# Kernel optimization log

Hardware: AMD Instinct MI355X
Metric: run time of the kernel (lower is better)

Reference implementation:

```python
import jax, jax.numpy as jnp
import numpy as np

N = 100000
E = 1600000
D_IN, D_HID, D_OUT = 256, 256, 128


def _sage_conv(x, src, dst, Wl, bl, Wr, n_nodes):
    # PyG SAGEConv (aggr='mean'): out = lin_l(mean_{j in N(i)} x_j) + lin_r(x_i)
    msg = x[src]                                               # [E, d]
    summed = jax.ops.segment_sum(msg, dst, num_segments=n_nodes)  # [N, d]
    deg = jax.ops.segment_sum(jnp.ones((src.shape[0],), x.dtype), dst,
                              num_segments=n_nodes)            # [N]
    agg = summed / jnp.maximum(deg, 1.0)[:, None]              # mean, 0 if isolated
    return agg @ Wl.T + bl + x @ Wr.T


def setup_inputs() -> dict:
    key = jax.random.key(0)
    ks = jax.random.split(key, 8)
    x = jax.random.normal(ks[0], (N, D_IN), dtype=jnp.float32)
    edge_index = jax.random.randint(ks[1], (2, E), 0, N, dtype=jnp.int32)
    s1 = 1.0 / np.sqrt(D_IN)
    s2 = 1.0 / np.sqrt(D_HID)
    W1l = jax.random.uniform(ks[2], (D_HID, D_IN), jnp.float32, -s1, s1)
    b1 = jnp.zeros((D_HID,), jnp.float32)
    W1r = jax.random.uniform(ks[3], (D_HID, D_IN), jnp.float32, -s1, s1)
    W2l = jax.random.uniform(ks[4], (D_OUT, D_HID), jnp.float32, -s2, s2)
    b2 = jnp.zeros((D_OUT,), jnp.float32)
    W2r = jax.random.uniform(ks[5], (D_OUT, D_HID), jnp.float32, -s2, s2)
    return {"x": x, "edge_index": edge_index, "W1l": W1l, "b1": b1,
            "W1r": W1r, "W2l": W2l, "b2": b2, "W2r": W2r}


def reference(x, edge_index, W1l, b1, W1r, W2l, b2, W2r):
    src, dst = edge_index[0], edge_index[1]
    h = _sage_conv(x, src, dst, W1l, b1, W1r, x.shape[0])
    h = jax.nn.relu(h)
    out = _sage_conv(h, src, dst, W2l, b2, W2r, x.shape[0])
    return out
```

## Files before the change

### kernel.cpp

```cpp
#include <hip/hip_runtime.h>

#define DK 256
#define BN 256
#define NBLK 512

typedef __attribute__((ext_vector_type(8))) short bf16x8;
typedef __attribute__((ext_vector_type(4))) float f32x4;

__device__ __forceinline__ unsigned short f2b(float f) {
    unsigned u = __builtin_bit_cast(unsigned, f);
    u += 0x7FFFu + ((u >> 16) & 1u);
    return (unsigned short)(u >> 16);
}
__device__ __forceinline__ float b2f(unsigned short s) {
    return __builtin_bit_cast(float, (unsigned)s << 16);
}
__device__ __forceinline__ void gld_lds16(void* lds, const void* g) {
    __builtin_amdgcn_global_load_lds(
        (const __attribute__((address_space(1))) unsigned int*)g,
        (__attribute__((address_space(3))) unsigned int*)lds, 16, 0, 0);
}

__global__ __launch_bounds__(256) void k_cvt(const float* __restrict__ src,
                                             unsigned short* __restrict__ dst, int n4) {
    int i = blockIdx.x * 256 + threadIdx.x;
    if (i < n4) {
        float4 v = reinterpret_cast<const float4*>(src)[i];
        ushort4 o = make_ushort4(f2b(v.x), f2b(v.y), f2b(v.z), f2b(v.w));
        reinterpret_cast<ushort4*>(dst)[i] = o;
    }
}

__global__ __launch_bounds__(256) void k_scan_a(const int* __restrict__ in,
                                                int* __restrict__ bsum, int N) {
    __shared__ int sm[256];
    int t = threadIdx.x;
    int i0 = blockIdx.x * 1024 + t * 4;
    int s = 0;
    if (i0 + 3 < N) {
        int4 v = *reinterpret_cast<const int4*>(in + i0);
        s = v.x + v.y + v.z + v.w;
    } else {
        for (int i = i0; i < min(i0 + 4, N); ++i) s += in[i];
    }
    sm[t] = s;
    __syncthreads();
    for (int off = 128; off > 0; off >>= 1) {
        if (t < off) sm[t] += sm[t + off];
        __syncthreads();
    }
    if (t == 0) bsum[blockIdx.x] = sm[0];
}

__global__ __launch_bounds__(256) void k_scan_b(const int* __restrict__ bsum,
                                                int* __restrict__ boff,
                                                int* __restrict__ totN, int NB) {
    __shared__ int sm[256];
    int t = threadIdx.x;
    sm[t] = (t < NB) ? bsum[t] : 0;
    __syncthreads();
    for (int off = 1; off < 256; off <<= 1) {
        int v = (t >= off) ? sm[t - off] : 0;
        __syncthreads();
        sm[t] += v;
        __syncthreads();
    }
    if (t < NB) boff[t] = (t == 0) ? 0 : sm[t - 1];
    if (t == NB - 1) *totN = sm[t];
}

__global__ __launch_bounds__(256) void k_scan_c(const int* __restrict__ in,
                                                const int* __restrict__ boff,
                                                int* __restrict__ rowptr,
                                                float* __restrict__ invdeg, int N) {
    __shared__ int sm[256];
    int t = threadIdx.x;
    int i0 = blockIdx.x * 1024 + t * 4;
    int d0 = 0, d1 = 0, d2 = 0, d3 = 0;
    if (i0 + 3 < N) {
        int4 v = *reinterpret_cast<const int4*>(in + i0);
        d0 = v.x; d1 = v.y; d2 = v.z; d3 = v.w;
    } else {
        if (i0 + 0 < N) d0 = in[i0 + 0];
        if (i0 + 1 < N) d1 = in[i0 + 1];
        if (i0 + 2 < N) d2 = in[i0 + 2];
        if (i0 + 3 < N) d3 = in[i0 + 3];
    }
    int s = d0 + d1 + d2 + d3;
    sm[t] = s;
    __syncthreads();
    for (int off = 1; off < 256; off <<= 1) {
        int v = (t >= off) ? sm[t - off] : 0;
        __syncthreads();
        sm[t] += v;
        __syncthreads();
    }
    int run = boff[blockIdx.x] + sm[t] - s;
    int dd[4] = {d0, d1, d2, d3};
#pragma unroll
    for (int i = 0; i < 4; ++i) {
        int idx = i0 + i;
        if (idx < N) {
            rowptr[idx] = run;
            invdeg[idx] = 1.0f / fmaxf((float)dd[i], 1.0f);
            run += dd[i];
        }
    }
}

__global__ __launch_bounds__(256) void k_scan_c2(const int* __restrict__ in,
                                                 const int* __restrict__ boff,
                                                 int* __restrict__ outx, int N) {
    __shared__ int sm[256];
    int t = threadIdx.x;
    int i0 = blockIdx.x * 1024 + t * 4;
    int d0 = 0, d1 = 0, d2 = 0, d3 = 0;
    if (i0 + 3 < N) {
        int4 v = *reinterpret_cast<const int4*>(in + i0);
        d0 = v.x; d1 = v.y; d2 = v.z; d3 = v.w;
    } else {
        if (i0 + 0 < N) d0 = in[i0 + 0];
        if (i0 + 1 < N) d1 = in[i0 + 1];
        if (i0 + 2 < N) d2 = in[i0 + 2];
        if (i0 + 3 < N) d3 = in[i0 + 3];
    }
    int s = d0 + d1 + d2 + d3;
    sm[t] = s;
    __syncthreads();
    for (int off = 1; off < 256; off <<= 1) {
        int v = (t >= off) ? sm[t - off] : 0;
        __syncthreads();
        sm[t] += v;
        __syncthreads();
    }
    int run = boff[blockIdx.x] + sm[t] - s;
    int dd[4] = {d0, d1, d2, d3};
#pragma unroll
    for (int i = 0; i < 4; ++i) {
        int idx = i0 + i;
        if (idx < N) { outx[idx] = run; run += dd[i]; }
    }
}

__global__ __launch_bounds__(256) void k_hist(const int* __restrict__ dst,
                                              int* __restrict__ hist,
                                              int E, int NBUK) {
    extern __shared__ int h[];
    int t = threadIdx.x;
    for (int b = t; b < NBUK; b += 256) h[b] = 0;
    __syncthreads();
    int CH = (E + NBLK - 1) / NBLK;
    int beg = blockIdx.x * CH;
    int end = min(beg + CH, E);
    for (int i = beg + t; i < end; i += 256)
        atomicAdd(&h[dst[i] >> 8], 1);
    __syncthreads();
    for (int b = t; b < NBUK; b += 256)
        hist[b * NBLK + blockIdx.x] = h[b];
}

__global__ __launch_bounds__(256) void k_part(const int* __restrict__ src,
                                              const int* __restrict__ dst,
                                              const int* __restrict__ hoff,
                                              unsigned* __restrict__ scratch,
                                              int E, int NBUK) {
    extern __shared__ int cur[];
    int t = threadIdx.x;
    for (int b = t; b < NBUK; b += 256) cur[b] = hoff[b * NBLK + blockIdx.x];
    __syncthreads();
    int CH = (E + NBLK - 1) / NBLK;
    int beg = blockIdx.x * CH;
    int end = min(beg + CH, E);
    for (int i = beg + t; i < end; i += 256) {
        int d = dst[i];
        int p = atomicAdd(&cur[d >> 8], 1);
        scratch[p] = (unsigned)src[i] | ((unsigned)(d & 255) << 20);
    }
}

__global__ __launch_bounds__(256) void k_degb(const unsigned* __restrict__ scratch,
                                              const int* __restrict__ hoff,
                                              int* __restrict__ degi,
                                              int E, int NBUK, int N) {
    __shared__ int cnt[BN];
    int b = blockIdx.x;
    int t = threadIdx.x;
    cnt[t] = 0;
    __syncthreads();
    int beg = hoff[b * NBLK];
    int end = (b + 1 < NBUK) ? hoff[(b + 1) * NBLK] : E;
    for (int i = beg + t; i < end; i += 256)
        atomicAdd(&cnt[scratch[i] >> 20], 1);
    __syncthreads();
    int node = b * BN + t;
    if (node < N) degi[node] = cnt[t];
}

__global__ __launch_bounds__(256) void k_scatter2(const unsigned* __restrict__ scratch,
                                                  const int* __restrict__ hoff,
                                                  const int* __restrict__ rowptr,
                                                  int* __restrict__ col,
                                                  int E, int NBUK, int N) {
    __shared__ int cur[BN];
    int b = blockIdx.x;
    int t = threadIdx.x;
    int node = b * BN + t;
    if (node < N) cur[t] = rowptr[node];
    __syncthreads();
    int beg = hoff[b * NBLK];
    int end = (b + 1 < NBUK) ? hoff[(b + 1) * NBLK] : E;
    for (int i = beg + t; i < end; i += 256) {
        unsigned v = scratch[i];
        int p = atomicAdd(&cur[v >> 20], 1);
        col[p] = (int)(v & 0xFFFFFu);
    }
}

template <bool RF32>
__global__ __launch_bounds__(256) void k_gemm_bf16(const unsigned short* __restrict__ A,
                                                   const unsigned short* __restrict__ W,
                                                   unsigned short* __restrict__ Y,
                                                   void* __restrict__ Rv,
                                                   int DOUTA, int N) {
    __shared__ unsigned short As[128 * 32];
    __shared__ unsigned short Bs[128 * 32];
    const int tid  = threadIdx.x;
    const int lane = tid & 63;
    const int w    = tid >> 6;
    const int wm   = w & 1, wn = w >> 1;
    const int m0   = blockIdx.x * 128;
    const int n0   = blockIdx.y * 128;
    const int lm   = lane & 15, quad = lane >> 4;

    f32x4 acc[4][4];
#pragma unroll
    for (int i = 0; i < 4; ++i)
#pragma unroll
        for (int j = 0; j < 4; ++j) acc[i][j] = (f32x4){0.f, 0.f, 0.f, 0.f};

    const int srow  = lane >> 2;
    const int skoff = (lane & 3) * 8;
    const int ca = 2 * w, cb = 2 * w + 1;

    for (int k0 = 0; k0 < DK; k0 += 32) {
        int ra = min(m0 + 16 * ca + srow, N - 1);
        int rb = min(m0 + 16 * cb + srow, N - 1);
        gld_lds16(As + ca * 512, A + (size_t)ra * DK + k0 + skoff);
        gld_lds16(As + cb * 512, A + (size_t)rb * DK + k0 + skoff);
        int na = n0 + 16 * ca + srow;
        int nb = n0 + 16 * cb + srow;
        gld_lds16(Bs + ca * 512, W + (size_t)na * DK + k0 + skoff);
        gld_lds16(Bs + cb * 512, W + (size_t)nb * DK + k0 + skoff);
        __syncthreads();

        bf16x8 af[4], bfr[4];
#pragma unroll
        for (int mt = 0; mt < 4; ++mt)
            af[mt] = *reinterpret_cast<const bf16x8*>(As + (wm * 64 + mt * 16 + lm) * 32 + quad * 8);
#pragma unroll
        for (int nt = 0; nt < 4; ++nt)
            bfr[nt] = *reinterpret_cast<const bf16x8*>(Bs + (wn * 64 + nt * 16 + lm) * 32 + quad * 8);
#pragma unroll
        for (int mt = 0; mt < 4; ++mt)
#pragma unroll
            for (int nt = 0; nt < 4; ++nt)
                acc[mt][nt] = __builtin_amdgcn_mfma_f32_16x16x32_bf16(af[mt], bfr[nt], acc[mt][nt], 0, 0, 0);
        __syncthreads();
    }

    const bool yPart = (n0 < DOUTA);
#pragma unroll
    for (int mt = 0; mt < 4; ++mt) {
#pragma unroll
        for (int nt = 0; nt < 4; ++nt) {
            int gn = n0 + wn * 64 + nt * 16 + lm;
#pragma unroll
            for (int reg = 0; reg < 4; ++reg) {
                int gm = m0 + wm * 64 + mt * 16 + quad * 4 + reg;
                if (gm < N) {
                    float v = acc[mt][nt][reg];
                    if (yPart) {
                        Y[(size_t)gm * DOUTA + gn] = f2b(v);
                    } else if (RF32) {
                        ((float*)Rv)[(size_t)gm * DOUTA + (gn - DOUTA)] = v;
                    } else {
                        ((unsigned short*)Rv)[(size_t)gm * DOUTA + (gn - DOUTA)] = f2b(v);
                    }
                }
            }
        }
    }
}

__global__ __launch_bounds__(256) void k_agg256(const unsigned short* __restrict__ Y,
                                                const unsigned short* __restrict__ Rb,
                                                const float* __restrict__ bias,
                                                const float* __restrict__ invdeg,
                                                const int* __restrict__ rowptr,
                                                const int* __restrict__ col,
                                                unsigned short* __restrict__ H, int N) {
    long long g = (long long)blockIdx.x * 256 + threadIdx.x;
    int node = (int)(g >> 6);
    int lane = (int)(g & 63);
    if (node >= N) return;
    int beg = rowptr[node], end = rowptr[node + 1];
    const unsigned short* yb = Y + lane * 4;
    float a0 = 0, a1 = 0, a2 = 0, a3 = 0;
    int e = beg;
    for (; e + 7 < end; e += 8) {
        int s[8];
#pragma unroll
        for (int u = 0; u < 8; ++u) s[u] = col[e + u];
        ushort4 v[8];
#pragma unroll
        for (int u = 0; u < 8; ++u)
            v[u] = *reinterpret_cast<const ushort4*>(yb + (size_t)s[u] * 256);
#pragma unroll
        for (int u = 0; u < 8; ++u) {
            a0 += b2f(v[u].x);
            a1 += b2f(v[u].y);
            a2 += b2f(v[u].z);
            a3 += b2f(v[u].w);
        }
    }
    for (; e < end; ++e) {
        ushort4 v0 = *reinterpret_cast<const ushort4*>(yb + (size_t)col[e] * 256);
        a0 += b2f(v0.x); a1 += b2f(v0.y); a2 += b2f(v0.z); a3 += b2f(v0.w);
    }
    float inv = invdeg[node];
    int c = lane * 4;
    ushort4 r = *reinterpret_cast<const ushort4*>(Rb + (size_t)node * 256 + c);
    float o0 = fmaxf(a0 * inv + bias[c + 0] + b2f(r.x), 0.f);
    float o1 = fmaxf(a1 * inv + bias[c + 1] + b2f(r.y), 0.f);
    float o2 = fmaxf(a2 * inv + bias[c + 2] + b2f(r.z), 0.f);
    float o3 = fmaxf(a3 * inv + bias[c + 3] + b2f(r.w), 0.f);
    *reinterpret_cast<ushort4*>(H + (size_t)node * 256 + c) =
        make_ushort4(f2b(o0), f2b(o1), f2b(o2), f2b(o3));
}

__global__ __launch_bounds__(256) void k_agg128(const unsigned short* __restrict__ Y,
                                                const float* __restrict__ Rf,
                                                const float* __restrict__ bias,
                                                const float* __restrict__ invdeg,
                                                const int* __restrict__ rowptr,
                                                const int* __restrict__ col,
                                                float* __restrict__ O, int N) {
    long long g = (long long)blockIdx.x * 256 + threadIdx.x;
    int node = (int)(g >> 6);
    int lane = (int)(g & 63);
    if (node >= N) return;
    int beg = rowptr[node], end = rowptr[node + 1];
    const unsigned short* yb = Y + lane * 2;
    float a0 = 0, a1 = 0;
    int e = beg;
    for (; e + 7 < end; e += 8) {
        int s[8];
#pragma unroll
        for (int u = 0; u < 8; ++u) s[u] = col[e + u];
        unsigned v[8];
#pragma unroll
        for (int u = 0; u < 8; ++u)
            v[u] = *reinterpret_cast<const unsigned*>(yb + (size_t)s[u] * 128);
#pragma unroll
        for (int u = 0; u < 8; ++u) {
            a0 += b2f((unsigned short)(v[u] & 0xffff));
            a1 += b2f((unsigned short)(v[u] >> 16));
        }
    }
    for (; e < end; ++e) {
        unsigned v0 = *reinterpret_cast<const unsigned*>(yb + (size_t)col[e] * 128);
        a0 += b2f((unsigned short)(v0 & 0xffff));
        a1 += b2f((unsigned short)(v0 >> 16));
    }
    float inv = invdeg[node];
    int c = lane * 2;
    float2 r = *reinterpret_cast<const float2*>(Rf + (size_t)node * 128 + c);
    float2 o;
    o.x = a0 * inv + bias[c + 0] + r.x;
    o.y = a1 * inv + bias[c + 1] + r.y;
    *reinterpret_cast<float2*>(O + (size_t)node * 128 + c) = o;
}

extern "C" void kernel_launch(void* const* d_in, const int* in_sizes, int n_in,
                              void* d_out, int out_size, void* d_ws, size_t ws_size,
                              hipStream_t stream) {
    const float* x   = (const float*)d_in[0];
    const int*   ei  = (const int*)d_in[1];
    const float* W1l = (const float*)d_in[2];
    const float* b1  = (const float*)d_in[3];
    const float* W1r = (const float*)d_in[4];
    const float* W2l = (const float*)d_in[5];
    const float* b2  = (const float*)d_in[6];
    const float* W2r = (const float*)d_in[7];
    float* out = (float*)d_out;

    const int N = in_sizes[0] / DK;
    const int E = in_sizes[1] / 2;
    const int* src = ei;
    const int* dst = ei + E;

    unsigned short* xb  = (unsigned short*)d_ws;
    unsigned short* y1b = xb + (size_t)N * 256;
    unsigned short* r1b = y1b + (size_t)N * 256;
    unsigned short* hb  = r1b + (size_t)N * 256;
    unsigned short* Wb1 = hb + (size_t)N * 256;
    unsigned short* Wb2 = Wb1 + 512 * 256;
    float* invdeg = (float*)(Wb2 + 256 * 256);
    int* degi   = (int*)(invdeg + N);
    int* rowptr = degi + N;
    int* col    = rowptr + (N + 1);
    int* bsum   = col + E;
    int* boff   = bsum + 512;
    unsigned short* y2b = y1b;
    float* r2f = (float*)r1b;

    const int NBUK = (N + BN - 1) / BN;
    const int NH   = NBUK * NBLK;
    unsigned* scratch = (unsigned*)hb;
    int* hist  = (int*)y1b;
    int* hoff  = hist + NH;
    int* bsum2 = hoff + NH;
    int* boff2 = bsum2 + 512;
    int* tot2  = boff2 + 512;

    k_cvt<<<(N * 64 + 255) / 256, 256, 0, stream>>>(x, xb, N * 64);
    k_cvt<<<(16384 + 255) / 256, 256, 0, stream>>>(W1l, Wb1, 16384);
    k_cvt<<<(16384 + 255) / 256, 256, 0, stream>>>(W1r, Wb1 + 256 * 256, 16384);
    k_cvt<<<(8192 + 255) / 256, 256, 0, stream>>>(W2l, Wb2, 8192);
    k_cvt<<<(8192 + 255) / 256, 256, 0, stream>>>(W2r, Wb2 + 128 * 256, 8192);

    const int NB2 = (NH + 1023) / 1024;
    const int NB  = (N + 1023) / 1024;
    k_hist<<<NBLK, 256, NBUK * sizeof(int), stream>>>(dst, hist, E, NBUK);
    k_scan_a<<<NB2, 256, 0, stream>>>(hist, bsum2, NH);
    k_scan_b<<<1, 256, 0, stream>>>(bsum2, boff2, tot2, NB2);
    k_scan_c2<<<NB2, 256, 0, stream>>>(hist, boff2, hoff, NH);
    k_part<<<NBLK, 256, NBUK * sizeof(int), stream>>>(src, dst, hoff, scratch, E, NBUK);
    k_degb<<<NBUK, 256, 0, stream>>>(scratch, hoff, degi, E, NBUK, N);
    k_scan_a<<<NB, 256, 0, stream>>>(degi, bsum, N);
    k_scan_b<<<1, 256, 0, stream>>>(bsum, boff, rowptr + N, NB);
    k_scan_c<<<NB, 256, 0, stream>>>(degi, boff, rowptr, invdeg, N);
    k_scatter2<<<NBUK, 256, 0, stream>>>(scratch, hoff, rowptr, col, E, NBUK, N);

    int mTiles = (N + 127) / 128;
    int aggBlocks = (N + 3) / 4;

    k_gemm_bf16<false><<<dim3(mTiles, 4), 256, 0, stream>>>(xb, Wb1, y1b, r1b, 256, N);
    k_agg256<<<aggBlocks, 256, 0, stream>>>(y1b, r1b, b1, invdeg, rowptr, col, hb, N);

    k_gemm_bf16<true><<<dim3(mTiles, 2), 256, 0, stream>>>(hb, Wb2, y2b, r2f, 128, N);
    k_agg128<<<aggBlocks, 256, 0, stream>>>(y2b, r2f, b2, invdeg, rowptr, col, out, N);
}
```

Measured before the change: 539.9 us.

## Widen aggregation loads with half-wave edge split, loop N-tiles in GEMM, merge weight casts

Both aggregation kernels now give each half-wave its own edges and use wider per-lane loads (16 bytes for the 256-wide layer, 8 bytes for the 128-wide one). The two halves are combined with a cross-half shuffle, and the bias and residual are read as vectors. The GEMMs drop the grid y-dimension and loop over output column tiles inside one block, so the A tile rows stay hot in cache across N-tiles, at the cost of fewer blocks. The four weight-conversion launches are merged into one kernel to cut launch overhead.

```diff
diff --git a/kernel.cpp b/kernel.cpp
--- a/kernel.cpp
+++ b/kernel.cpp
@@ -29,6 +29,24 @@
         ushort4 o = make_ushort4(f2b(v.x), f2b(v.y), f2b(v.z), f2b(v.w));
         reinterpret_cast<ushort4*>(dst)[i] = o;
     }
+}
+
+__global__ __launch_bounds__(256) void k_cvtw(const float* __restrict__ a,
+                                              const float* __restrict__ b,
+                                              const float* __restrict__ c,
+                                              const float* __restrict__ d,
+                                              unsigned short* __restrict__ Wb1,
+                                              unsigned short* __restrict__ Wb2) {
+    int i = blockIdx.x * 256 + threadIdx.x;
+    const float* s;
+    unsigned short* o;
+    if (i < 16384)      { s = a; o = Wb1; }
+    else if (i < 32768) { s = b; o = Wb1 + 256 * 256; i -= 16384; }
+    else if (i < 40960) { s = c; o = Wb2;             i -= 32768; }
+    else                { s = d; o = Wb2 + 128 * 256; i -= 40960; }
+    float4 v = reinterpret_cast<const float4*>(s)[i];
+    ushort4 w = make_ushort4(f2b(v.x), f2b(v.y), f2b(v.z), f2b(v.w));
+    reinterpret_cast<ushort4*>(o)[i] = w;
 }
 
 __global__ __launch_bounds__(256) void k_scan_a(const int* __restrict__ in,
@@ -216,12 +234,12 @@
     }
 }
 
-template <bool RF32>
+template <bool RF32, int NT>
 __global__ __launch_bounds__(256) void k_gemm_bf16(const unsigned short* __restrict__ A,
                                                    const unsigned short* __restrict__ W,
                                                    unsigned short* __restrict__ Y,
-                                                   void* __restrict__ Rv,
-                                                   int DOUTA, int N) {
+                                                   void* __restrict__ Rv, int N) {
+    constexpr int DOUTA = NT * 64;
     __shared__ unsigned short As[128 * 32];
     __shared__ unsigned short Bs[128 * 32];
     const int tid  = threadIdx.x;
@@ -229,62 +247,64 @@
     const int w    = tid >> 6;
     const int wm   = w & 1, wn = w >> 1;
     const int m0   = blockIdx.x * 128;
-    const int n0   = blockIdx.y * 128;
     const int lm   = lane & 15, quad = lane >> 4;
-
-    f32x4 acc[4][4];
-#pragma unroll
-    for (int i = 0; i < 4; ++i)
-#pragma unroll
-        for (int j = 0; j < 4; ++j) acc[i][j] = (f32x4){0.f, 0.f, 0.f, 0.f};
 
     const int srow  = lane >> 2;
     const int skoff = (lane & 3) * 8;
     const int ca = 2 * w, cb = 2 * w + 1;
 
-    for (int k0 = 0; k0 < DK; k0 += 32) {
-        int ra = min(m0 + 16 * ca + srow, N - 1);
-        int rb = min(m0 + 16 * cb + srow, N - 1);
-        gld_lds16(As + ca * 512, A + (size_t)ra * DK + k0 + skoff);
-        gld_lds16(As + cb * 512, A + (size_t)rb * DK + k0 + skoff);
-        int na = n0 + 16 * ca + srow;
-        int nb = n0 + 16 * cb + srow;
-        gld_lds16(Bs + ca * 512, W + (size_t)na * DK + k0 + skoff);
-        gld_lds16(Bs + cb * 512, W + (size_t)nb * DK + k0 + skoff);
-        __syncthreads();
-
-        bf16x8 af[4], bfr[4];
-#pragma unroll
-        for (int mt = 0; mt < 4; ++mt)
-            af[mt] = *reinterpret_cast<const bf16x8*>(As + (wm * 64 + mt * 16 + lm) * 32 + quad * 8);
-#pragma unroll
-        for (int nt = 0; nt < 4; ++nt)
-            bfr[nt] = *reinterpret_cast<const bf16x8*>(Bs + (wn * 64 + nt * 16 + lm) * 32 + quad * 8);
-#pragma unroll
-        for (int mt = 0; mt < 4; ++mt)
-#pragma unroll
-            for (int nt = 0; nt < 4; ++nt)
-                acc[mt][nt] = __builtin_amdgcn_mfma_f32_16x16x32_bf16(af[mt], bfr[nt], acc[mt][nt], 0, 0, 0);
-        __syncthreads();
-    }
-
-    const bool yPart = (n0 < DOUTA);
-#pragma unroll
-    for (int mt = 0; mt < 4; ++mt) {
-#pragma unroll
-        for (int nt = 0; nt < 4; ++nt) {
-            int gn = n0 + wn * 64 + nt * 16 + lm;
-#pragma unroll
-            for (int reg = 0; reg < 4; ++reg) {
-                int gm = m0 + wm * 64 + mt * 16 + quad * 4 + reg;
-                if (gm < N) {
-                    float v = acc[mt][nt][reg];
-                    if (yPart) {
-                        Y[(size_t)gm * DOUTA + gn] = f2b(v);
-                    } else if (RF32) {
-                        ((float*)Rv)[(size_t)gm * DOUTA + (gn - DOUTA)] = v;
-                    } else {
-                        ((unsigned short*)Rv)[(size_t)gm * DOUTA + (gn - DOUTA)] = f2b(v);
+    for (int nt = 0; nt < NT; ++nt) {
+        const int n0 = nt * 128;
+        f32x4 acc[4][4];
+#pragma unroll
+        for (int i = 0; i < 4; ++i)
+#pragma unroll
+            for (int j = 0; j < 4; ++j) acc[i][j] = (f32x4){0.f, 0.f, 0.f, 0.f};
+
+        for (int k0 = 0; k0 < DK; k0 += 32) {
+            int ra = min(m0 + 16 * ca + srow, N - 1);
+            int rb = min(m0 + 16 * cb + srow, N - 1);
+            gld_lds16(As + ca * 512, A + (size_t)ra * DK + k0 + skoff);
+            gld_lds16(As + cb * 512, A + (size_t)rb * DK + k0 + skoff);
+            int na = n0 + 16 * ca + srow;
+            int nb = n0 + 16 * cb + srow;
+            gld_lds16(Bs + ca * 512, W + (size_t)na * DK + k0 + skoff);
+            gld_lds16(Bs + cb * 512, W + (size_t)nb * DK + k0 + skoff);
+            __syncthreads();
+
+            bf16x8 af[4], bfr[4];
+#pragma unroll
+            for (int mt = 0; mt < 4; ++mt)
+                af[mt] = *reinterpret_cast<const bf16x8*>(As + (wm * 64 + mt * 16 + lm) * 32 + quad * 8);
+#pragma unroll
+            for (int ntf = 0; ntf < 4; ++ntf)
+                bfr[ntf] = *reinterpret_cast<const bf16x8*>(Bs + (wn * 64 + ntf * 16 + lm) * 32 + quad * 8);
+#pragma unroll
+            for (int mt = 0; mt < 4; ++mt)
+#pragma unroll
+                for (int ntf = 0; ntf < 4; ++ntf)
+                    acc[mt][ntf] = __builtin_amdgcn_mfma_f32_16x16x32_bf16(af[mt], bfr[ntf], acc[mt][ntf], 0, 0, 0);
+            __syncthreads();
+        }
+
+        const bool yPart = (n0 < DOUTA);
+#pragma unroll
+        for (int mt = 0; mt < 4; ++mt) {
+#pragma unroll
+            for (int ntf = 0; ntf < 4; ++ntf) {
+                int gn = n0 + wn * 64 + ntf * 16 + lm;
+#pragma unroll
+                for (int reg = 0; reg < 4; ++reg) {
+                    int gm = m0 + wm * 64 + mt * 16 + quad * 4 + reg;
+                    if (gm < N) {
+                        float v = acc[mt][ntf][reg];
+                        if (yPart) {
+                            Y[(size_t)gm * DOUTA + gn] = f2b(v);
+                        } else if (RF32) {
+                            ((float*)Rv)[(size_t)gm * DOUTA + (gn - DOUTA)] = v;
+                        } else {
+                            ((unsigned short*)Rv)[(size_t)gm * DOUTA + (gn - DOUTA)] = f2b(v);
+                        }
                     }
                 }
             }
@@ -299,43 +319,59 @@
                                                 const int* __restrict__ rowptr,
                                                 const int* __restrict__ col,
                                                 unsigned short* __restrict__ H, int N) {
-    long long g = (long long)blockIdx.x * 256 + threadIdx.x;
-    int node = (int)(g >> 6);
-    int lane = (int)(g & 63);
+    int g = blockIdx.x * 256 + threadIdx.x;
+    int node = g >> 6;
+    int lane = g & 63;
     if (node >= N) return;
+    int half = lane >> 5, sub = lane & 31;
     int beg = rowptr[node], end = rowptr[node + 1];
-    const unsigned short* yb = Y + lane * 4;
-    float a0 = 0, a1 = 0, a2 = 0, a3 = 0;
+    const unsigned short* yb = Y + sub * 8;
+    float a[8];
+#pragma unroll
+    for (int j = 0; j < 8; ++j) a[j] = 0.f;
     int e = beg;
     for (; e + 7 < end; e += 8) {
-        int s[8];
-#pragma unroll
-        for (int u = 0; u < 8; ++u) s[u] = col[e + u];
-        ushort4 v[8];
-#pragma unroll
-        for (int u = 0; u < 8; ++u)
-            v[u] = *reinterpret_cast<const ushort4*>(yb + (size_t)s[u] * 256);
-#pragma unroll
-        for (int u = 0; u < 8; ++u) {
-            a0 += b2f(v[u].x);
-            a1 += b2f(v[u].y);
-            a2 += b2f(v[u].z);
-            a3 += b2f(v[u].w);
+        int s[4];
+#pragma unroll
+        for (int u = 0; u < 4; ++u) s[u] = col[e + 2 * u + half];
+        bf16x8 v[4];
+#pragma unroll
+        for (int u = 0; u < 4; ++u)
+            v[u] = *reinterpret_cast<const bf16x8*>(yb + (size_t)s[u] * 256);
+#pragma unroll
+        for (int u = 0; u < 4; ++u)
+#pragma unroll
+            for (int j = 0; j < 8; ++j) a[j] += b2f((unsigned short)v[u][j]);
+    }
+    for (; e + 1 < end; e += 2) {
+        int s0 = col[e + half];
+        bf16x8 v0 = *reinterpret_cast<const bf16x8*>(yb + (size_t)s0 * 256);
+#pragma unroll
+        for (int j = 0; j < 8; ++j) a[j] += b2f((unsigned short)v0[j]);
+    }
+    if (e < end && half == 0) {
+        int s0 = col[e];
+        bf16x8 v0 = *reinterpret_cast<const bf16x8*>(yb + (size_t)s0 * 256);
+#pragma unroll
+        for (int j = 0; j < 8; ++j) a[j] += b2f((unsigned short)v0[j]);
+    }
+#pragma unroll
+    for (int j = 0; j < 8; ++j) a[j] += __shfl_xor(a[j], 32);
+    if (half == 0) {
+        float inv = invdeg[node];
+        int c = sub * 8;
+        bf16x8 r = *reinterpret_cast<const bf16x8*>(Rb + (size_t)node * 256 + c);
+        f32x4 b0 = *reinterpret_cast<const f32x4*>(bias + c);
+        f32x4 b1v = *reinterpret_cast<const f32x4*>(bias + c + 4);
+        bf16x8 o;
+#pragma unroll
+        for (int j = 0; j < 8; ++j) {
+            float bj = (j < 4) ? b0[j] : b1v[j - 4];
+            float ov = fmaxf(a[j] * inv + bj + b2f((unsigned short)r[j]), 0.f);
+            o[j] = (short)f2b(ov);
         }
-    }
-    for (; e < end; ++e) {
-        ushort4 v0 = *reinterpret_cast<const ushort4*>(yb + (size_t)col[e] * 256);
-        a0 += b2f(v0.x); a1 += b2f(v0.y); a2 += b2f(v0.z); a3 += b2f(v0.w);
-    }
-    float inv = invdeg[node];
-    int c = lane * 4;
-    ushort4 r = *reinterpret_cast<const ushort4*>(Rb + (size_t)node * 256 + c);
-    float o0 = fmaxf(a0 * inv + bias[c + 0] + b2f(r.x), 0.f);
-    float o1 = fmaxf(a1 * inv + bias[c + 1] + b2f(r.y), 0.f);
-    float o2 = fmaxf(a2 * inv + bias[c + 2] + b2f(r.z), 0.f);
-    float o3 = fmaxf(a3 * inv + bias[c + 3] + b2f(r.w), 0.f);
-    *reinterpret_cast<ushort4*>(H + (size_t)node * 256 + c) =
-        make_ushort4(f2b(o0), f2b(o1), f2b(o2), f2b(o3));
+        *reinterpret_cast<bf16x8*>(H + (size_t)node * 256 + c) = o;
+    }
 }
 
 __global__ __launch_bounds__(256) void k_agg128(const unsigned short* __restrict__ Y,
@@ -345,40 +381,55 @@
                                                 const int* __restrict__ rowptr,
                                                 const int* __restrict__ col,
                                                 float* __restrict__ O, int N) {
-    long long g = (long long)blockIdx.x * 256 + threadIdx.x;
-    int node = (int)(g >> 6);
-    int lane = (int)(g & 63);
+    int g = blockIdx.x * 256 + threadIdx.x;
+    int node = g >> 6;
+    int lane = g & 63;
     if (node >= N) return;
+    int half = lane >> 5, sub = lane & 31;
     int beg = rowptr[node], end = rowptr[node + 1];
-    const unsigned short* yb = Y + lane * 2;
-    float a0 = 0, a1 = 0;
+    const unsigned short* yb = Y + sub * 4;
+    float a0 = 0, a1 = 0, a2 = 0, a3 = 0;
     int e = beg;
     for (; e + 7 < end; e += 8) {
-        int s[8];
-#pragma unroll
-        for (int u = 0; u < 8; ++u) s[u] = col[e + u];
-        unsigned v[8];
-#pragma unroll
-        for (int u = 0; u < 8; ++u)
-            v[u] = *reinterpret_cast<const unsigned*>(yb + (size_t)s[u] * 128);
-#pragma unroll
-        for (int u = 0; u < 8; ++u) {
-            a0 += b2f((unsigned short)(v[u] & 0xffff));
-            a1 += b2f((unsigned short)(v[u] >> 16));
+        int s[4];
+#pragma unroll
+        for (int u = 0; u < 4; ++u) s[u] = col[e + 2 * u + half];
+        ushort4 v[4];
+#pragma unroll
+        for (int u = 0; u < 4; ++u)
+            v[u] = *reinterpret_cast<const ushort4*>(yb + (size_t)s[u] * 128);
+#pragma unroll
+        for (int u = 0; u < 4; ++u) {
+            a0 += b2f(v[u].x); a1 += b2f(v[u].y);
+            a2 += b2f(v[u].z); a3 += b2f(v[u].w);
         }
     }
-    for (; e < end; ++e) {
-        unsigned v0 = *reinterpret_cast<const unsigned*>(yb + (size_t)col[e] * 128);
-        a0 += b2f((unsigned short)(v0 & 0xffff));
-        a1 += b2f((unsigned short)(v0 >> 16));
-    }
-    float inv = invdeg[node];
-    int c = lane * 2;
-    float2 r = *reinterpret_cast<const float2*>(Rf + (size_t)node * 128 + c);
-    float2 o;
-    o.x = a0 * inv + bias[c + 0] + r.x;
-    o.y = a1 * inv + bias[c + 1] + r.y;
-    *reinterpret_cast<float2*>(O + (size_t)node * 128 + c) = o;
+    for (; e + 1 < end; e += 2) {
+        int s0 = col[e + half];
+        ushort4 v0 = *reinterpret_cast<const ushort4*>(yb + (size_t)s0 * 128);
+        a0 += b2f(v0.x); a1 += b2f(v0.y); a2 += b2f(v0.z); a3 += b2f(v0.w);
+    }
+    if (e < end && half == 0) {
+        int s0 = col[e];
+        ushort4 v0 = *reinterpret_cast<const ushort4*>(yb + (size_t)s0 * 128);
+        a0 += b2f(v0.x); a1 += b2f(v0.y); a2 += b2f(v0.z); a3 += b2f(v0.w);
+    }
+    a0 += __shfl_xor(a0, 32);
+    a1 += __shfl_xor(a1, 32);
+    a2 += __shfl_xor(a2, 32);
+    a3 += __shfl_xor(a3, 32);
+    if (half == 0) {
+        float inv = invdeg[node];
+        int c = sub * 4;
+        f32x4 r = *reinterpret_cast<const f32x4*>(Rf + (size_t)node * 128 + c);
+        f32x4 bv = *reinterpret_cast<const f32x4*>(bias + c);
+        f32x4 o;
+        o[0] = a0 * inv + bv[0] + r[0];
+        o[1] = a1 * inv + bv[1] + r[1];
+        o[2] = a2 * inv + bv[2] + r[2];
+        o[3] = a3 * inv + bv[3] + r[3];
+        *reinterpret_cast<f32x4*>(O + (size_t)node * 128 + c) = o;
+    }
 }
 
 extern "C" void kernel_launch(void* const* d_in, const int* in_sizes, int n_in,
@@ -424,10 +475,7 @@
     int* tot2  = boff2 + 512;
 
     k_cvt<<<(N * 64 + 255) / 256, 256, 0, stream>>>(x, xb, N * 64);
-    k_cvt<<<(16384 + 255) / 256, 256, 0, stream>>>(W1l, Wb1, 16384);
-    k_cvt<<<(16384 + 255) / 256, 256, 0, stream>>>(W1r, Wb1 + 256 * 256, 16384);
-    k_cvt<<<(8192 + 255) / 256, 256, 0, stream>>>(W2l, Wb2, 8192);
-    k_cvt<<<(8192 + 255) / 256, 256, 0, stream>>>(W2r, Wb2 + 128 * 256, 8192);
+    k_cvtw<<<192, 256, 0, stream>>>(W1l, W1r, W2l, W2r, Wb1, Wb2);
 
     const int NB2 = (NH + 1023) / 1024;
     const int NB  = (N + 1023) / 1024;
@@ -445,9 +493,9 @@
     int mTiles = (N + 127) / 128;
     int aggBlocks = (N + 3) / 4;
 
-    k_gemm_bf16<false><<<dim3(mTiles, 4), 256, 0, stream>>>(xb, Wb1, y1b, r1b, 256, N);
+    k_gemm_bf16<false, 4><<<mTiles, 256, 0, stream>>>(xb, Wb1, y1b, r1b, N);
     k_agg256<<<aggBlocks, 256, 0, stream>>>(y1b, r1b, b1, invdeg, rowptr, col, hb, N);
 
-    k_gemm_bf16<true><<<dim3(mTiles, 2), 256, 0, stream>>>(hb, Wb2, y2b, r2f, 128, N);
+    k_gemm_bf16<true, 2><<<mTiles, 256, 0, stream>>>(hb, Wb2, y2b, r2f, N);
     k_agg128<<<aggBlocks, 256, 0, stream>>>(y2b, r2f, b2, invdeg, rowptr, col, out, N);
 }
```

New measurement: 541.7 us. No clear change (+0.3%).
